# Performance work log

Measured on AMD Instinct MI355X. Metric: run time of the kernel, lower is better.

## Reference

```python
import jax, jax.numpy as jnp
import numpy as np

N_NODES = 20000
N_EDGES = 320000
N_GRAPHS = 64
D = 128  # node_dim


def _gat_conv(h, W, al, ar, b, src, dst, n, res=None, act=None):
    # DGL GATConv: fc -> per-head attn logits -> leaky_relu -> edge softmax per dst -> scatter-add
    H, Dh = al.shape
    feat = (h @ W).reshape(n, H, Dh)                      # [N,H,D]
    el = jnp.einsum('nhd,hd->nh', feat, al)               # [N,H]
    er = jnp.einsum('nhd,hd->nh', feat, ar)               # [N,H]
    e = jax.nn.leaky_relu(el[src] + er[dst], 0.2)         # [E,H]
    m = jax.ops.segment_max(e, dst, num_segments=n)       # [N,H]
    m = jnp.where(jnp.isfinite(m), m, 0.0)
    a = jnp.exp(e - m[dst])                               # [E,H]
    den = jax.ops.segment_sum(a, dst, num_segments=n)     # [N,H]
    a = a / jnp.maximum(den, 1e-9)[dst]
    out = jax.ops.segment_sum(a[:, :, None] * feat[src], dst, num_segments=n)  # [N,H,D]
    if res is not None:
        out = out + res
    out = out + b.reshape(1, H, Dh)
    return act(out) if act is not None else out


def setup_inputs() -> dict:
    key = jax.random.key(0)
    ks = jax.random.split(key, 20)
    s = 0.05
    inp = {
        'h': jax.random.normal(ks[0], (N_NODES, D), jnp.float32),
        'he': jax.random.normal(ks[1], (N_EDGES, 64), jnp.float32),
        'src': jax.random.randint(ks[2], (N_EDGES,), 0, N_NODES),
        'dst': jax.random.randint(ks[3], (N_EDGES,), 0, N_NODES),
        'graph_id': jnp.sort(jax.random.randint(ks[4], (N_NODES,), 0, N_GRAPHS)),
        # layer 0: in=D, heads=4, out=D
        'W0': jax.random.normal(ks[5], (D, 4 * D), jnp.float32) * s,
        'al0': jax.random.normal(ks[6], (4, D), jnp.float32) * s,
        'ar0': jax.random.normal(ks[7], (4, D), jnp.float32) * s,
        'b0': jnp.zeros((4 * D,), jnp.float32),
        # layer 1: in=4D, heads=4, out=D, residual (identity since 4D==4*D)
        'W1': jax.random.normal(ks[8], (4 * D, 4 * D), jnp.float32) * s,
        'al1': jax.random.normal(ks[9], (4, D), jnp.float32) * s,
        'ar1': jax.random.normal(ks[10], (4, D), jnp.float32) * s,
        'b1': jnp.zeros((4 * D,), jnp.float32),
        # layer 2: in=4D, heads=6, out=D, residual via res_fc (4D -> 6D)
        'W2': jax.random.normal(ks[11], (4 * D, 6 * D), jnp.float32) * s,
        'al2': jax.random.normal(ks[12], (6, D), jnp.float32) * s,
        'ar2': jax.random.normal(ks[13], (6, D), jnp.float32) * s,
        'b2': jnp.zeros((6 * D,), jnp.float32),
        'resW2': jax.random.normal(ks[14], (4 * D, 6 * D), jnp.float32) * s,
        # final MLP (1 layer): Linear(D, D)
        'Wm': jax.random.normal(ks[15], (D, D), jnp.float32) * s,
        'bm': jnp.zeros((D,), jnp.float32),
    }
    return inp


def reference(h, he, src, dst, graph_id, W0, al0, ar0, b0, W1, al1, ar1, b1,
              W2, al2, ar2, b2, resW2, Wm, bm):
    n = h.shape[0]
    elu = jax.nn.elu
    # layer 0 (no residual, elu), flatten heads
    x = _gat_conv(h, W0, al0, ar0, b0, src, dst, n, res=None, act=elu)
    x = x.reshape(n, -1)  # [N, 4D]
    # layer 1 (identity residual, elu), flatten heads
    res1 = x.reshape(n, 4, D)
    x2 = _gat_conv(x, W1, al1, ar1, b1, src, dst, n, res=res1, act=elu)
    x2 = x2.reshape(n, -1)  # [N, 4D]
    # layer 2 (linear residual, no activation), mean over heads
    res2 = (x2 @ resW2).reshape(n, 6, D)
    x3 = _gat_conv(x2, W2, al2, ar2, b2, src, dst, n, res=res2, act=None)
    local_feat = x3.mean(axis=1)  # [N, D]
    # avg pooling per graph + linear
    sums = jax.ops.segment_sum(local_feat, graph_id, num_segments=N_GRAPHS)
    cnts = jax.ops.segment_sum(jnp.ones((n,), local_feat.dtype), graph_id, num_segments=N_GRAPHS)
    pooled = sums / jnp.maximum(cnts, 1.0)[:, None]  # [G, D]
    global_feat = pooled @ Wm + bm
    return (local_feat, global_feat)
```

## Files before the change

### kernel.cpp

```cpp
#include <hip/hip_runtime.h>
#include <math.h>


typedef _Float16 f16;
typedef __attribute__((ext_vector_type(8))) _Float16 half8;
typedef __attribute__((ext_vector_type(4))) _Float16 half4;
typedef __attribute__((ext_vector_type(4))) float float4v;

union U16 { unsigned short u; _Float16 h; };

#define M_PAD 20096
#define CHSTRIDE ((size_t)M_PAD * 64)

__device__ inline void gload_lds16(const void* g, void* l) {
    __builtin_amdgcn_global_load_lds((const __attribute__((address_space(1))) unsigned*)g,
                                     (__attribute__((address_space(3))) unsigned*)l,
                                     16, 0, 0);
}


__global__ __launch_bounds__(256) void deg_kernel(const int* __restrict__ dst,
                                                  int* __restrict__ deg, int E) {
    int e = blockIdx.x * 256 + threadIdx.x;
    if (e < E) atomicAdd(&deg[dst[e]], 1);
}

__global__ __launch_bounds__(1024) void scan_kernel(const int* __restrict__ deg,
                                                    int* __restrict__ row_off,
                                                    const int* __restrict__ gid,
                                                    int* __restrict__ gstart, int n) {
    __shared__ int sums[1024];
    int t = threadIdx.x;
    if (t <= 64) {
        int g = t, lo = 0, hi = n;
        while (lo < hi) {
            int mid = (lo + hi) >> 1;
            if (gid[mid] < g) lo = mid + 1; else hi = mid;
        }
        gstart[g] = lo;
    }
    int CH = (n + 1023) >> 10;
    int base = t * CH;
    int s = 0;
    for (int i = 0; i < CH; ++i) { int idx = base + i; if (idx < n) s += deg[idx]; }
    sums[t] = s;
    __syncthreads();
    for (int off = 1; off < 1024; off <<= 1) {
        int v = (t >= off) ? sums[t - off] : 0;
        __syncthreads();
        sums[t] += v;
        __syncthreads();
    }
    int run = (t == 0) ? 0 : sums[t - 1];
    for (int i = 0; i < CH; ++i) {
        int idx = base + i;
        if (idx < n) { row_off[idx] = run; run += deg[idx]; }
    }
    if (t == 1023) row_off[n] = run;
}

__global__ __launch_bounds__(256) void fill_kernel(const int* __restrict__ src,
                                                   const int* __restrict__ dst,
                                                   const int* __restrict__ row_off,
                                                   int* __restrict__ fill,
                                                   int* __restrict__ csr_src, int E) {
    int e = blockIdx.x * 256 + threadIdx.x;
    if (e < E) {
        int d = dst[e];
        int pos = row_off[d] + atomicAdd(&fill[d], 1);
        csr_src[pos] = src[e];
    }
}


__global__ __launch_bounds__(256) void prep_kernel(
        const float* __restrict__ h, f16* __restrict__ h16,
        f16* __restrict__ x1, f16* __restrict__ x2,
        const float* __restrict__ W0, f16* __restrict__ Wt0,
        const float* __restrict__ W1, f16* __restrict__ Wt1,
        const float* __restrict__ W2, const float* __restrict__ resW2,
        f16* __restrict__ Wt2cat,
        int* __restrict__ deg2, int n) {
    __shared__ float tile[32][33];
    int b = blockIdx.x;
    int t = threadIdx.x;
    if (b < 2512) {
        long i = ((long)b * 256 + t) * 4;
        long nv = (long)n * 128;
        float4 v = make_float4(0.f, 0.f, 0.f, 0.f);
        if (i < nv) v = *(const float4*)&h[i];
        half4 o; o[0] = (f16)v.x; o[1] = (f16)v.y; o[2] = (f16)v.z; o[3] = (f16)v.w;
        *(half4*)&h16[i] = o;
        return;
    }
    b -= 2512;
    if (b < 48) {
        int idx = (b * 256 + t) * 4;
        int total = (M_PAD - n) * 512;
        if (idx < total) {
            half4 z; z[0] = (f16)0.f; z[1] = (f16)0.f; z[2] = (f16)0.f; z[3] = (f16)0.f;
            *(half4*)&x1[(size_t)n * 512 + idx] = z;
            *(half4*)&x2[(size_t)n * 512 + idx] = z;
        }
        return;
    }
    b -= 48;
    {
        const float* W = nullptr; f16* Wt = nullptr;
        int K = 0, N = 0, bx = 0, by = 0;
        bool dotr = false;
        if (b < 64)        { W = W0; Wt = Wt0;    K = 128; N = 512; bx = b & 15;  by = b >> 4; dotr = true; }
        else if (b < 320)  { int r = b - 64;  W = W1; Wt = Wt1;    K = 512; N = 512; bx = r & 15;  by = r >> 4; dotr = true; }
        else if (b < 704)  { int r = b - 320; W = W2; Wt = Wt2cat; K = 512; N = 768; bx = r % 24;  by = r / 24; dotr = true; }
        if (dotr) {
            int tx = t & 31, ty = t >> 5;
            int n0 = bx * 32, k0 = by * 32;
#pragma unroll
            for (int i = 0; i < 32; i += 8)
                tile[ty + i][tx] = W[(size_t)(k0 + ty + i) * N + n0 + tx];
            __syncthreads();
#pragma unroll
            for (int i = 0; i < 32; i += 8)
                Wt[(size_t)(n0 + ty + i) * K + k0 + tx] = (f16)tile[tx][ty + i];
            return;
        }
    }
    b -= 704;
    if (b < 256) {
        int idx = b * 256 + t;
        int d = idx >> 9;
        int k = idx & 511;
        float s = 0.f;
#pragma unroll
        for (int hh = 0; hh < 6; ++hh) s += resW2[(size_t)k * 768 + hh * 128 + d];
        Wt2cat[(size_t)(768 + d) * 512 + k] = (f16)(s * (1.f / 6.f));
        return;
    }
    b -= 256;
    {
        int idx = (b * 256 + t) * 4;
        if (idx < 2 * n) *(int4*)&deg2[idx] = make_int4(0, 0, 0, 0);
    }
}


#define STAGE(buf, k0) do {                                   \
    f16* a_ = As + (buf) * 2048 + t * 8;                      \
    f16* b_ = Bs + (buf) * 4096 + t * 8;                      \
    gload_lds16(ag0 + (k0), a_);                              \
    gload_lds16(bg0 + (k0), b_);                              \
    gload_lds16(bg1 + (k0), b_ + 2048);                       \
} while (0)

__global__ __launch_bounds__(256) void gemm16_kernel(const f16* __restrict__ A,
                                                     const f16* __restrict__ Bt,
                                                     f16* __restrict__ Cc,
                                                     f16* __restrict__ Cr,
                                                     const float* __restrict__ al,
                                                     const float* __restrict__ ar,
                                                     float* __restrict__ el8,
                                                     float* __restrict__ er8,
                                                     int N, int K, int nchunk,
                                                     int nheads, int nvalid) {
    __shared__ f16 As[2 * 64 * 32];
    __shared__ f16 Bs[2 * 128 * 32];
    __shared__ float elds[2][2][64];
    int t = threadIdx.x;
    int w = t >> 6;
    int l = t & 63;

    int gx = gridDim.x;
    int nwg = gx * gridDim.y;
    int wg = blockIdx.y * gx + blockIdx.x;
    int qq = nwg >> 3, rr = nwg & 7;
    int xcd = wg & 7, idx = wg >> 3;
    int swz = (xcd < rr ? xcd * (qq + 1) : rr * (qq + 1) + (xcd - rr) * qq) + idx;
    int bxi = swz % gx;
    int byi = swz / gx;

    size_t bm = (size_t)byi * 64;
    int bn = bxi * 128;
    int wm = (w & 1) * 32;
    int wn = (w >> 1) * 64;

    int srow = t >> 2;
    int sq = (t & 3) ^ ((srow >> 1) & 3);
    const f16* ag0 = A + (bm + srow) * K + sq * 8;
    const f16* bg0 = Bt + (size_t)(bn + srow) * K + sq * 8;
    const f16* bg1 = Bt + (size_t)(bn + 64 + srow) * K + sq * 8;

    float4v acc[2][4];
#pragma unroll
    for (int i = 0; i < 2; ++i)
#pragma unroll
        for (int j = 0; j < 4; ++j) acc[i][j] = (float4v)(0.f);

    int ml = l & 15, q = l >> 4;
    int sslot = (q ^ ((ml >> 1) & 3)) * 8;
    int apoff = (wm + ml) * 32 + sslot;
    int bpoff = (wn + ml) * 32 + sslot;

    STAGE(0, 0);
    __syncthreads();
    int cur = 0;
    for (int k0 = 0; k0 < K; k0 += 32) {
        if (k0 + 32 < K) STAGE(cur ^ 1, k0 + 32);
        const f16* ap = As + cur * 2048 + apoff;
        const f16* bp = Bs + cur * 4096 + bpoff;
        half8 af[2], bf[4];
#pragma unroll
        for (int mt = 0; mt < 2; ++mt) af[mt] = *(const half8*)(ap + mt * 16 * 32);
#pragma unroll
        for (int nt = 0; nt < 4; ++nt) bf[nt] = *(const half8*)(bp + nt * 16 * 32);
#pragma unroll
        for (int mt = 0; mt < 2; ++mt)
#pragma unroll
            for (int nt = 0; nt < 4; ++nt)
                acc[mt][nt] = __builtin_amdgcn_mfma_f32_16x16x32_f16(bf[nt], af[mt],
                                                                     acc[mt][nt], 0, 0, 0);
        __syncthreads();
        cur ^= 1;
    }
#pragma unroll
    for (int mt = 0; mt < 2; ++mt) {
        size_t row = bm + wm + mt * 16 + ml;
#pragma unroll
        for (int nt = 0; nt < 4; ++nt) {
            half4 hv;
#pragma unroll
            for (int r = 0; r < 4; ++r) hv[r] = (f16)acc[mt][nt][r];
            int col = bn + wn + nt * 16 + q * 4;
            if (col < nchunk) {
                *(half4*)&Cc[(size_t)(col >> 6) * CHSTRIDE + row * 64 + (col & 63)] = hv;
            } else {
                *(half4*)&Cr[row * (size_t)(N - nchunk) + (col - nchunk)] = hv;
            }
        }
    }
    if (al != nullptr && bn < nheads * 128) {
        int hh = bn >> 7;
        float4 a4[4], r4[4];
#pragma unroll
        for (int nt = 0; nt < 4; ++nt) {
            int ci = hh * 128 + wn + nt * 16 + q * 4;
            a4[nt] = *(const float4*)&al[ci];
            r4[nt] = *(const float4*)&ar[ci];
        }
        int wnidx = wn >> 6;
#pragma unroll
        for (int mt = 0; mt < 2; ++mt) {
            float ep = 0.f, rp = 0.f;
#pragma unroll
            for (int nt = 0; nt < 4; ++nt) {
                ep += acc[mt][nt][0] * a4[nt].x + acc[mt][nt][1] * a4[nt].y
                    + acc[mt][nt][2] * a4[nt].z + acc[mt][nt][3] * a4[nt].w;
                rp += acc[mt][nt][0] * r4[nt].x + acc[mt][nt][1] * r4[nt].y
                    + acc[mt][nt][2] * r4[nt].z + acc[mt][nt][3] * r4[nt].w;
            }
            ep += __shfl_xor(ep, 16, 64); ep += __shfl_xor(ep, 32, 64);
            rp += __shfl_xor(rp, 16, 64); rp += __shfl_xor(rp, 32, 64);
            if (q == 0) {
                elds[0][wnidx][wm + mt * 16 + ml] = ep;
                elds[1][wnidx][wm + mt * 16 + ml] = rp;
            }
        }
        __syncthreads();
        if (((t >> 6) & 1) == 0) {
            int row = t & 63, which = t >> 7;
            long gv = (long)bm + row;
            if (gv < nvalid) {
                float vs = elds[which][0][row] + elds[which][1][row];
                if (which == 0) el8[gv * 8 + hh] = vs;
                else            er8[gv * 8 + hh] = vs;
            }
        }
    }
}


__global__ __launch_bounds__(256, 8) void edge_weight_kernel(
        const float* __restrict__ el8, const float* __restrict__ er8,
        const int* __restrict__ row_off, const int* __restrict__ csr_src,
        int* __restrict__ wp, float* __restrict__ inv8,
        int H, int n, int E) {
    int wid = threadIdx.x >> 6, lane = threadIdx.x & 63;
    int c2 = lane >> 4;
    int sl = lane & 15;
    int v = blockIdx.x * 16 + wid * 4 + c2;
    if (v >= n) return;
    float era[6];
    {
        float4 a = *(const float4*)&er8[(size_t)v * 8];
        float2 b = *(const float2*)&er8[(size_t)v * 8 + 4];
        era[0] = a.x; era[1] = a.y; era[2] = a.z; era[3] = a.w;
        era[4] = b.x; era[5] = b.y;
    }
    int beg = row_off[v], end = row_off[v + 1];
    float lsum[6] = {0.f, 0.f, 0.f, 0.f, 0.f, 0.f};
    for (int pos = beg; pos < end; pos += 16) {
        int cnt = min(16, end - pos);
        int s_l = (sl < cnt) ? csr_src[pos + sl] : 0;
        float4 a = *(const float4*)&el8[(size_t)s_l * 8];
        float2 bq = *(const float2*)&el8[(size_t)s_l * 8 + 4];
        float ee[6] = {a.x, a.y, a.z, a.w, bq.x, bq.y};
#pragma unroll
        for (int h = 0; h < 6; ++h) {
            if (h < H) {
                float lg = ee[h] + era[h];
                lg = (lg >= 0.f) ? lg : 0.2f * lg;
                float wv = __expf(lg);
                if (sl >= cnt) wv = 0.f;
                lsum[h] += wv;
                if (sl < cnt) {
                    U16 uu; uu.h = (f16)wv;
                    wp[(size_t)h * E + pos + sl] = s_l | ((int)uu.u << 16);
                }
            }
        }
    }
#pragma unroll
    for (int h = 0; h < 6; ++h)
#pragma unroll
        for (int off = 8; off >= 1; off >>= 1)
            lsum[h] += __shfl_xor(lsum[h], off, 64);
    if (sl == 0) {
#pragma unroll
        for (int h = 0; h < 6; ++h)
            if (h < H) inv8[(size_t)v * 8 + h] = 1.f / fmaxf(lsum[h], 1e-9f);
    }
}


__device__ __forceinline__ void agg_chunk_body(
        const f16* __restrict__ fc, const int* __restrict__ wp,
        const float* __restrict__ inv8, int head,
        const int* __restrict__ row_off,
        const f16* __restrict__ res, const float* __restrict__ bias,
        f16* __restrict__ out16, float* __restrict__ out32,
        int n, int width, int act, int chunk,
        int wave_id, int wavestride, int lane) {
    int c = lane >> 3;
    int j = lane & 7;
    int coff = j * 8;
    int cb = chunk * 64 + coff;
    float4 bv0 = *(const float4*)&bias[cb];
    float4 bv1 = *(const float4*)&bias[cb + 4];
    int clbase = lane & 56;

    for (int v0 = wave_id * 8; v0 < n; v0 += wavestride * 8) {
        int v = v0 + c;
        bool valid = (v < n);
        int beg = 0, end = 0;
        if (valid) { beg = row_off[v]; end = row_off[v + 1]; }
        int rounds = end - beg;
        rounds = max(rounds, __shfl_xor(rounds, 8, 64));
        rounds = max(rounds, __shfl_xor(rounds, 16, 64));
        rounds = max(rounds, __shfl_xor(rounds, 32, 64));
        float acc[8] = {0.f, 0.f, 0.f, 0.f, 0.f, 0.f, 0.f, 0.f};
        int pidx = beg + j;
        int pk = (pidx < end) ? wp[pidx] : 0;
        for (int base = 0; base < rounds; base += 8) {
            int pn = beg + base + 8 + j;
            int pk_nxt = (pn < end) ? wp[pn] : 0;
#pragma unroll
            for (int hg = 0; hg < 2; ++hg) {
                int cb4 = clbase + hg * 4;
                int p0 = __shfl(pk, cb4 + 0, 64);
                int p1 = __shfl(pk, cb4 + 1, 64);
                int p2 = __shfl(pk, cb4 + 2, 64);
                int p3 = __shfl(pk, cb4 + 3, 64);
                half8 f0 = *(const half8*)&fc[(size_t)(p0 & 0xFFFF) * 64 + coff];
                half8 f1 = *(const half8*)&fc[(size_t)(p1 & 0xFFFF) * 64 + coff];
                half8 f2 = *(const half8*)&fc[(size_t)(p2 & 0xFFFF) * 64 + coff];
                half8 f3 = *(const half8*)&fc[(size_t)(p3 & 0xFFFF) * 64 + coff];
                U16 u0; u0.u = (unsigned short)((unsigned)p0 >> 16); float w0 = (float)u0.h;
                U16 u1; u1.u = (unsigned short)((unsigned)p1 >> 16); float w1 = (float)u1.h;
                U16 u2; u2.u = (unsigned short)((unsigned)p2 >> 16); float w2 = (float)u2.h;
                U16 u3; u3.u = (unsigned short)((unsigned)p3 >> 16); float w3 = (float)u3.h;
#pragma unroll
                for (int k = 0; k < 8; ++k) acc[k] += w0 * (float)f0[k];
#pragma unroll
                for (int k = 0; k < 8; ++k) acc[k] += w1 * (float)f1[k];
#pragma unroll
                for (int k = 0; k < 8; ++k) acc[k] += w2 * (float)f2[k];
#pragma unroll
                for (int k = 0; k < 8; ++k) acc[k] += w3 * (float)f3[k];
            }
            pk = pk_nxt;
        }
        if (valid) {
            float inv = inv8[(size_t)v * 8 + head];
            float ox[8];
#pragma unroll
            for (int k = 0; k < 8; ++k) ox[k] = acc[k] * inv;
            size_t base = (size_t)v * width + cb;
            if (res) {
                half8 rr = *(const half8*)&res[base];
#pragma unroll
                for (int k = 0; k < 8; ++k) ox[k] += (float)rr[k];
            }
            ox[0] += bv0.x; ox[1] += bv0.y; ox[2] += bv0.z; ox[3] += bv0.w;
            ox[4] += bv1.x; ox[5] += bv1.y; ox[6] += bv1.z; ox[7] += bv1.w;
            if (act) {
#pragma unroll
                for (int k = 0; k < 8; ++k)
                    ox[k] = (ox[k] > 0.f) ? ox[k] : expm1f(ox[k]);
            }
            if (out16) {
                half8 o;
#pragma unroll
                for (int k = 0; k < 8; ++k) o[k] = (f16)ox[k];
                *(half8*)&out16[base] = o;
            } else {
                *(float4*)&out32[base]     = make_float4(ox[0], ox[1], ox[2], ox[3]);
                *(float4*)&out32[base + 4] = make_float4(ox[4], ox[5], ox[6], ox[7]);
            }
        }
    }
}

__global__ __launch_bounds__(256, 6) void agg_chunk_kernel(
        const f16* __restrict__ featc, const int* __restrict__ wp,
        const float* __restrict__ inv8,
        const int* __restrict__ row_off,
        const f16* __restrict__ res, const float* __restrict__ bias,
        f16* __restrict__ out16, float* __restrict__ out32,
        int n, int nchunks, int width, int E, int act) {
    int wid = threadIdx.x >> 6, lane = threadIdx.x & 63;
    int b = blockIdx.x;
    {
        int chunk = b & 7;
        agg_chunk_body(featc + (size_t)chunk * CHSTRIDE, wp + (size_t)(chunk >> 1) * E,
                       inv8, chunk >> 1, row_off, res, bias, out16, out32,
                       n, width, act, chunk, (b >> 3) * 4 + wid, 1024, lane);
    }
    if (nchunks > 8) {
        int chunk = 8 + (b & 3);
        if (chunk < nchunks)
            agg_chunk_body(featc + (size_t)chunk * CHSTRIDE, wp + (size_t)(chunk >> 1) * E,
                           inv8, chunk >> 1, row_off, res, bias, out16, out32,
                           n, width, act, chunk, (b >> 2) * 4 + wid, 2048, lane);
    }
}


__global__ __launch_bounds__(128) void mean_pool_kernel(const float* __restrict__ x3,
                                                        const f16* __restrict__ resm,
                                                        float* __restrict__ local, int n) {
    int v = blockIdx.x;
    int d = threadIdx.x;
    const float* p = x3 + (size_t)v * 768;
    float s = 0.f;
#pragma unroll
    for (int h = 0; h < 6; ++h) s += p[h * 128 + d];
    local[(size_t)v * 128 + d] = s * (1.f / 6.f) + (float)resm[(size_t)v * 128 + d];
}


__global__ __launch_bounds__(1024) void graph_pool_kernel(const float* __restrict__ local,
                                                          const int* __restrict__ gstart,
                                                          const float* __restrict__ Wm,
                                                          const float* __restrict__ bm,
                                                          float* __restrict__ gout) {
    __shared__ float buf[8][128];
    __shared__ float p[128];
    int g = blockIdx.x;
    int t = threadIdx.x;
    int c = t & 127;
    int sub = t >> 7;
    int beg = gstart[g], end = gstart[g + 1];
    float s = 0.f;
    for (int v = beg + sub; v < end; v += 8) s += local[(size_t)v * 128 + c];
    buf[sub][c] = s;
    __syncthreads();
    if (sub == 0) {
        float tot = 0.f;
#pragma unroll
        for (int k = 0; k < 8; ++k) tot += buf[k][c];
        float cntf = fmaxf((float)(end - beg), 1.f);
        p[c] = tot / cntf;
    }
    __syncthreads();
    if (t < 128) {
        float s2 = 0.f;
#pragma unroll 16
        for (int k = 0; k < 128; ++k) s2 += p[k] * Wm[k * 128 + t];
        gout[g * 128 + t] = s2 + bm[t];
    }
}


extern "C" void kernel_launch(void* const* d_in, const int* in_sizes, int n_in,
                              void* d_out, int out_size, void* d_ws, size_t ws_size,
                              hipStream_t stream) {
    const float* h     = (const float*)d_in[0];
    const int*   src   = (const int*)d_in[2];
    const int*   dst   = (const int*)d_in[3];
    const int*   gid   = (const int*)d_in[4];
    const float* W0    = (const float*)d_in[5];
    const float* al0   = (const float*)d_in[6];
    const float* ar0   = (const float*)d_in[7];
    const float* b0    = (const float*)d_in[8];
    const float* W1    = (const float*)d_in[9];
    const float* al1   = (const float*)d_in[10];
    const float* ar1   = (const float*)d_in[11];
    const float* b1    = (const float*)d_in[12];
    const float* W2    = (const float*)d_in[13];
    const float* al2   = (const float*)d_in[14];
    const float* ar2   = (const float*)d_in[15];
    const float* b2    = (const float*)d_in[16];
    const float* resW2 = (const float*)d_in[17];
    const float* Wm    = (const float*)d_in[18];
    const float* bm    = (const float*)d_in[19];

    const int n = in_sizes[0] / 128;
    const int E = in_sizes[2];

    size_t off = 0;
    auto take = [&](size_t bytes) -> void* {
        void* p = (char*)d_ws + off;
        off = (off + bytes + 255) & ~(size_t)255;
        return p;
    };
    f16* h16     = (f16*)take((size_t)M_PAD * 128 * 2);
    f16* Wt0     = (f16*)take((size_t)512 * 128 * 2);
    f16* Wt1     = (f16*)take((size_t)512 * 512 * 2);
    f16* Wt2cat  = (f16*)take((size_t)896 * 512 * 2);
    f16* featc   = (f16*)take((size_t)12 * CHSTRIDE * 2);
    f16* resm    = (f16*)take((size_t)M_PAD * 128 * 2);
    f16* x1_16   = (f16*)take((size_t)M_PAD * 512 * 2);
    f16* x2_16   = (f16*)take((size_t)M_PAD * 512 * 2);
    float* x3    = (float*)take((size_t)n * 768 * 4);
    int* wp      = (int*)take((size_t)6 * E * 4);
    float* inv8  = (float*)take((size_t)n * 8 * 4);
    float* el8   = (float*)take((size_t)n * 8 * 4);
    float* er8   = (float*)take((size_t)n * 8 * 4);
    int* deg     = (int*)take((size_t)2 * n * 4);
    int* fillc   = deg + n;
    int* row_off = (int*)take((size_t)(n + 1) * 4);
    int* csr_src = (int*)take((size_t)E * 4);
    int* gstart  = (int*)take(65 * 4);

    float* out_local  = (float*)d_out;
    float* out_global = (float*)d_out + (size_t)n * 128;

    prep_kernel<<<3560, 256, 0, stream>>>(h, h16, x1_16, x2_16, W0, Wt0, W1, Wt1,
                                          W2, resW2, Wt2cat, deg, n);

    deg_kernel<<<(E + 255) / 256, 256, 0, stream>>>(dst, deg, E);
    scan_kernel<<<1, 1024, 0, stream>>>(deg, row_off, gid, gstart, n);
    fill_kernel<<<(E + 255) / 256, 256, 0, stream>>>(src, dst, row_off, fillc, csr_src, E);

    const int gy = M_PAD / 64;
    const int ew_blocks = (n + 15) / 16;

    gemm16_kernel<<<dim3(512 / 128, gy), 256, 0, stream>>>(h16, Wt0, featc, nullptr,
                                                           al0, ar0, el8, er8, 512, 128, 512, 4, n);
    edge_weight_kernel<<<ew_blocks, 256, 0, stream>>>(el8, er8, row_off, csr_src, wp, inv8, 4, n, E);
    agg_chunk_kernel<<<2048, 256, 0, stream>>>(featc, wp, inv8, row_off,
                                               nullptr, b0, x1_16, nullptr, n, 8, 512, E, 1);
    gemm16_kernel<<<dim3(512 / 128, gy), 256, 0, stream>>>(x1_16, Wt1, featc, nullptr,
                                                           al1, ar1, el8, er8, 512, 512, 512, 4, n);
    edge_weight_kernel<<<ew_blocks, 256, 0, stream>>>(el8, er8, row_off, csr_src, wp, inv8, 4, n, E);
    agg_chunk_kernel<<<2048, 256, 0, stream>>>(featc, wp, inv8, row_off,
                                               x1_16, b1, x2_16, nullptr, n, 8, 512, E, 1);
    gemm16_kernel<<<dim3(896 / 128, gy), 256, 0, stream>>>(x2_16, Wt2cat, featc, resm,
                                                           al2, ar2, el8, er8, 896, 512, 768, 6, n);
    edge_weight_kernel<<<ew_blocks, 256, 0, stream>>>(el8, er8, row_off, csr_src, wp, inv8, 6, n, E);
    agg_chunk_kernel<<<2048, 256, 0, stream>>>(featc, wp, inv8, row_off,
                                               nullptr, b2, nullptr, x3, n, 12, 768, E, 0);
    mean_pool_kernel<<<n, 128, 0, stream>>>(x3, resm, out_local, n);
    graph_pool_kernel<<<64, 1024, 0, stream>>>(out_local, gstart, Wm, bm, out_global);
}
```

Measured before the change: 504.9 us.

## Fuse edge-weight computation into aggregation kernel, drop wp/inv8 buffers

Removes the separate edge_weight_kernel and computes the attention logit, leaky-relu, exp and per-destination sum inside the aggregation loop, gathering el8 per source on the fly. This eliminates three launches and the write/read of the packed weight array and the inverse-sum array. In exchange each of the two channel chunks per head recomputes the exps and gathers el8 redundantly, and an extra dependent gather sits in the prefetch path. The per-destination normalisation is now done with a lane shuffle reduction.

```diff
diff --git a/kernel.cpp b/kernel.cpp
--- a/kernel.cpp
+++ b/kernel.cpp
@@ -278,62 +278,9 @@
 }
 
 
-__global__ __launch_bounds__(256, 8) void edge_weight_kernel(
-        const float* __restrict__ el8, const float* __restrict__ er8,
-        const int* __restrict__ row_off, const int* __restrict__ csr_src,
-        int* __restrict__ wp, float* __restrict__ inv8,
-        int H, int n, int E) {
-    int wid = threadIdx.x >> 6, lane = threadIdx.x & 63;
-    int c2 = lane >> 4;
-    int sl = lane & 15;
-    int v = blockIdx.x * 16 + wid * 4 + c2;
-    if (v >= n) return;
-    float era[6];
-    {
-        float4 a = *(const float4*)&er8[(size_t)v * 8];
-        float2 b = *(const float2*)&er8[(size_t)v * 8 + 4];
-        era[0] = a.x; era[1] = a.y; era[2] = a.z; era[3] = a.w;
-        era[4] = b.x; era[5] = b.y;
-    }
-    int beg = row_off[v], end = row_off[v + 1];
-    float lsum[6] = {0.f, 0.f, 0.f, 0.f, 0.f, 0.f};
-    for (int pos = beg; pos < end; pos += 16) {
-        int cnt = min(16, end - pos);
-        int s_l = (sl < cnt) ? csr_src[pos + sl] : 0;
-        float4 a = *(const float4*)&el8[(size_t)s_l * 8];
-        float2 bq = *(const float2*)&el8[(size_t)s_l * 8 + 4];
-        float ee[6] = {a.x, a.y, a.z, a.w, bq.x, bq.y};
-#pragma unroll
-        for (int h = 0; h < 6; ++h) {
-            if (h < H) {
-                float lg = ee[h] + era[h];
-                lg = (lg >= 0.f) ? lg : 0.2f * lg;
-                float wv = __expf(lg);
-                if (sl >= cnt) wv = 0.f;
-                lsum[h] += wv;
-                if (sl < cnt) {
-                    U16 uu; uu.h = (f16)wv;
-                    wp[(size_t)h * E + pos + sl] = s_l | ((int)uu.u << 16);
-                }
-            }
-        }
-    }
-#pragma unroll
-    for (int h = 0; h < 6; ++h)
-#pragma unroll
-        for (int off = 8; off >= 1; off >>= 1)
-            lsum[h] += __shfl_xor(lsum[h], off, 64);
-    if (sl == 0) {
-#pragma unroll
-        for (int h = 0; h < 6; ++h)
-            if (h < H) inv8[(size_t)v * 8 + h] = 1.f / fmaxf(lsum[h], 1e-9f);
-    }
-}
-
-
 __device__ __forceinline__ void agg_chunk_body(
-        const f16* __restrict__ fc, const int* __restrict__ wp,
-        const float* __restrict__ inv8, int head,
+        const f16* __restrict__ fc, const int* __restrict__ csr_src,
+        const float* __restrict__ el8, const float* __restrict__ er8, int head,
         const int* __restrict__ row_off,
         const f16* __restrict__ res, const float* __restrict__ bias,
         f16* __restrict__ out16, float* __restrict__ out32,
@@ -356,12 +303,36 @@
         rounds = max(rounds, __shfl_xor(rounds, 8, 64));
         rounds = max(rounds, __shfl_xor(rounds, 16, 64));
         rounds = max(rounds, __shfl_xor(rounds, 32, 64));
+        float erv = valid ? er8[(size_t)v * 8 + head] : 0.f;
         float acc[8] = {0.f, 0.f, 0.f, 0.f, 0.f, 0.f, 0.f, 0.f};
-        int pidx = beg + j;
-        int pk = (pidx < end) ? wp[pidx] : 0;
+        float lsum = 0.f;
+        int pk;
+        {
+            int pidx = beg + j;
+            bool ok = pidx < end;
+            int s = ok ? csr_src[pidx] : 0;
+            float el = ok ? el8[(size_t)s * 8 + head] : 0.f;
+            float lg = el + erv;
+            lg = (lg >= 0.f) ? lg : 0.2f * lg;
+            float wv = ok ? __expf(lg) : 0.f;
+            lsum += wv;
+            U16 uu; uu.h = (f16)wv;
+            pk = s | ((int)uu.u << 16);
+        }
         for (int base = 0; base < rounds; base += 8) {
-            int pn = beg + base + 8 + j;
-            int pk_nxt = (pn < end) ? wp[pn] : 0;
+            int pk_nxt;
+            {
+                int pn = beg + base + 8 + j;
+                bool ok = pn < end;
+                int s = ok ? csr_src[pn] : 0;
+                float el = ok ? el8[(size_t)s * 8 + head] : 0.f;
+                float lg = el + erv;
+                lg = (lg >= 0.f) ? lg : 0.2f * lg;
+                float wv = ok ? __expf(lg) : 0.f;
+                lsum += wv;
+                U16 uu; uu.h = (f16)wv;
+                pk_nxt = s | ((int)uu.u << 16);
+            }
 #pragma unroll
             for (int hg = 0; hg < 2; ++hg) {
                 int cb4 = clbase + hg * 4;
@@ -388,8 +359,11 @@
             }
             pk = pk_nxt;
         }
+        lsum += __shfl_xor(lsum, 1, 64);
+        lsum += __shfl_xor(lsum, 2, 64);
+        lsum += __shfl_xor(lsum, 4, 64);
         if (valid) {
-            float inv = inv8[(size_t)v * 8 + head];
+            float inv = 1.f / fmaxf(lsum, 1e-9f);
             float ox[8];
 #pragma unroll
             for (int k = 0; k < 8; ++k) ox[k] = acc[k] * inv;
@@ -420,8 +394,8 @@
 }
 
 __global__ __launch_bounds__(256, 6) void agg_chunk_kernel(
-        const f16* __restrict__ featc, const int* __restrict__ wp,
-        const float* __restrict__ inv8,
+        const f16* __restrict__ featc, const int* __restrict__ csr_src,
+        const float* __restrict__ el8, const float* __restrict__ er8,
         const int* __restrict__ row_off,
         const f16* __restrict__ res, const float* __restrict__ bias,
         f16* __restrict__ out16, float* __restrict__ out32,
@@ -430,15 +404,15 @@
     int b = blockIdx.x;
     {
         int chunk = b & 7;
-        agg_chunk_body(featc + (size_t)chunk * CHSTRIDE, wp + (size_t)(chunk >> 1) * E,
-                       inv8, chunk >> 1, row_off, res, bias, out16, out32,
+        agg_chunk_body(featc + (size_t)chunk * CHSTRIDE, csr_src, el8, er8,
+                       chunk >> 1, row_off, res, bias, out16, out32,
                        n, width, act, chunk, (b >> 3) * 4 + wid, 1024, lane);
     }
     if (nchunks > 8) {
         int chunk = 8 + (b & 3);
         if (chunk < nchunks)
-            agg_chunk_body(featc + (size_t)chunk * CHSTRIDE, wp + (size_t)(chunk >> 1) * E,
-                           inv8, chunk >> 1, row_off, res, bias, out16, out32,
+            agg_chunk_body(featc + (size_t)chunk * CHSTRIDE, csr_src, el8, er8,
+                           chunk >> 1, row_off, res, bias, out16, out32,
                            n, width, act, chunk, (b >> 2) * 4 + wid, 2048, lane);
     }
 }
@@ -531,8 +505,6 @@
     f16* x1_16   = (f16*)take((size_t)M_PAD * 512 * 2);
     f16* x2_16   = (f16*)take((size_t)M_PAD * 512 * 2);
     float* x3    = (float*)take((size_t)n * 768 * 4);
-    int* wp      = (int*)take((size_t)6 * E * 4);
-    float* inv8  = (float*)take((size_t)n * 8 * 4);
     float* el8   = (float*)take((size_t)n * 8 * 4);
     float* er8   = (float*)take((size_t)n * 8 * 4);
     int* deg     = (int*)take((size_t)2 * n * 4);
@@ -552,22 +524,18 @@
     fill_kernel<<<(E + 255) / 256, 256, 0, stream>>>(src, dst, row_off, fillc, csr_src, E);
 
     const int gy = M_PAD / 64;
-    const int ew_blocks = (n + 15) / 16;
 
     gemm16_kernel<<<dim3(512 / 128, gy), 256, 0, stream>>>(h16, Wt0, featc, nullptr,
                                                            al0, ar0, el8, er8, 512, 128, 512, 4, n);
-    edge_weight_kernel<<<ew_blocks, 256, 0, stream>>>(el8, er8, row_off, csr_src, wp, inv8, 4, n, E);
-    agg_chunk_kernel<<<2048, 256, 0, stream>>>(featc, wp, inv8, row_off,
+    agg_chunk_kernel<<<2048, 256, 0, stream>>>(featc, csr_src, el8, er8, row_off,
                                                nullptr, b0, x1_16, nullptr, n, 8, 512, E, 1);
     gemm16_kernel<<<dim3(512 / 128, gy), 256, 0, stream>>>(x1_16, Wt1, featc, nullptr,
                                                            al1, ar1, el8, er8, 512, 512, 512, 4, n);
-    edge_weight_kernel<<<ew_blocks, 256, 0, stream>>>(el8, er8, row_off, csr_src, wp, inv8, 4, n, E);
-    agg_chunk_kernel<<<2048, 256, 0, stream>>>(featc, wp, inv8, row_off,
+    agg_chunk_kernel<<<2048, 256, 0, stream>>>(featc, csr_src, el8, er8, row_off,
                                                x1_16, b1, x2_16, nullptr, n, 8, 512, E, 1);
     gemm16_kernel<<<dim3(896 / 128, gy), 256, 0, stream>>>(x2_16, Wt2cat, featc, resm,
                                                            al2, ar2, el8, er8, 896, 512, 768, 6, n);
-    edge_weight_kernel<<<ew_blocks, 256, 0, stream>>>(el8, er8, row_off, csr_src, wp, inv8, 6, n, E);
-    agg_chunk_kernel<<<2048, 256, 0, stream>>>(featc, wp, inv8, row_off,
+    agg_chunk_kernel<<<2048, 256, 0, stream>>>(featc, csr_src, el8, er8, row_off,
                                                nullptr, b2, nullptr, x3, n, 12, 768, E, 0);
     mean_pool_kernel<<<n, 128, 0, stream>>>(x3, resm, out_local, n);
     graph_pool_kernel<<<64, 1024, 0, stream>>>(out_local, gstart, Wm, bm, out_global);
```

After: 548.1 us. +8.6%, slower.
